# Kernel tuning notes

Hardware: AMD Instinct MI355X
Metric: run time of the kernel (lower is better)

Reference implementation:

```python
import jax, jax.numpy as jnp
import numpy as np

B, LQ, LD = 64, 20, 512
D, NB, WIN = 300, 11, 5
EQ, ED, DESC, KC = 5, 10, 20, 10
VW, VE, VC = 50000, 10000, 5000

# KNRM kernel centers / widths (requires_grad=False buffers in the original)
MU = jnp.array([1.0, 0.9, 0.7, 0.5, 0.3, 0.1, -0.1, -0.3, -0.5, -0.7, -0.9], jnp.float32)
SIGMA = jnp.array([1e-3] + [0.1] * 10, jnp.float32)


def setup_inputs() -> dict:
    key = jax.random.key(0)
    ks = jax.random.split(key, 20)
    f = lambda k, s, sc: jax.random.normal(k, s, jnp.float32) * sc
    return {
        "inputs_qwt": jax.random.randint(ks[0], (B, LQ), 0, VW),
        "inputs_qwm": jnp.ones((B, LQ), jnp.float32),
        "inputs_qei": jax.random.randint(ks[1], (B, EQ), 0, VE),
        "inputs_qet": jax.random.randint(ks[2], (B, EQ * DESC), 0, VW),
        "inputs_qew": jax.random.randint(ks[3], (B, EQ * KC), 0, VC),
        "inputs_qem": jnp.ones((B, EQ), jnp.float32),
        "inputs_dwt": jax.random.randint(ks[4], (B, LD), 0, VW),
        "inputs_dwm": jnp.ones((B, LD), jnp.float32),
        "inputs_dei": jax.random.randint(ks[5], (B, ED), 0, VE),
        "inputs_det": jax.random.randint(ks[6], (B, ED * DESC), 0, VW),
        "inputs_dew": jax.random.randint(ks[7], (B, ED * KC), 0, VC),
        "inputs_dem": jnp.ones((B, ED), jnp.float32),
        "wrd_emb": f(ks[8], (VW, D), 0.1),
        "ent_emb": f(ks[9], (VE, 128), 0.1),
        "car_emb": f(ks[10], (VC, 128), 0.1),
        "bow_W": f(ks[11], (128, D), 0.05), "bow_b": jnp.zeros((128,), jnp.float32),
        "conv_uni_W": f(ks[12], (128, 1, D), 0.05), "conv_uni_b": jnp.zeros((128,), jnp.float32),
        "conv_bi_W": f(ks[13], (128, 2, D), 0.04), "conv_bi_b": jnp.zeros((128,), jnp.float32),
        "conv_tri_W": f(ks[14], (128, 3, D), 0.03), "conv_tri_b": jnp.zeros((128,), jnp.float32),
        "conv_des_W": f(ks[15], (128, WIN, D), 0.02), "conv_des_b": jnp.zeros((128,), jnp.float32),
        "dense_f_W": f(ks[16], (1, 16 * NB), 0.1), "dense_f_b": jnp.zeros((1,), jnp.float32),
    }


def _conv_words(x, w, b):
    # x: [N, L, D]; w: [O, k, D] -> relu conv over the word axis, valid padding -> [N, L-k+1, O]
    k, L = w.shape[1], x.shape[1]
    segs = jnp.stack([x[:, i:L - k + 1 + i] for i in range(k)], axis=2)  # [N, L-k+1, k, D]
    return jax.nn.relu(jnp.einsum('nlkd,okd->nlo', segs, w) + b)


def _l2(x):
    return x / jnp.maximum(jnp.linalg.norm(x, axis=-1, keepdims=True), 1e-10)


def _kernel_pool(q, d, mq, md):
    # q:[B,Lq,128] d:[B,Ld,128] mq:[B,Lq] md:[B,Ld] -> [B, NB]
    sim = jnp.einsum('bqe,bde->bqd', q, d)
    pv = jnp.exp(-0.5 * (sim[..., None] - MU) ** 2 / (SIGMA ** 2)) * md[:, None, :, None]
    lps = jnp.log(jnp.maximum(pv.sum(2), 1e-10)) * 0.01 * mq[:, :, None]
    return lps.sum(1)


def _forward(inputs_qwt, inputs_qwm, inputs_qei, inputs_qet, inputs_qew, inputs_qem,
             inputs_dwt, inputs_dwm, inputs_dei, inputs_det, inputs_dew, inputs_dem,
             wrd_emb, ent_emb, car_emb, bow_W, bow_b,
             conv_uni_W, conv_uni_b, conv_bi_W, conv_bi_b, conv_tri_W, conv_tri_b,
             conv_des_W, conv_des_b, dense_f_W, dense_f_b):
    b = inputs_qwt.shape[0]
    qw = wrd_emb[inputs_qwt]  # [B, LQ, D]
    dw = wrd_emb[inputs_dwt]  # [B, LD, D]

    def ent_branch(ids_e, ids_desc, ids_car, n_ent, w_bow):
        desc = wrd_emb[ids_desc].reshape(b * n_ent, DESC, D)
        e_conv = _conv_words(desc, conv_des_W, conv_des_b).max(1).reshape(b, n_ent, 128)
        t = car_emb[ids_car].reshape(b, n_ent * KC, 128)
        att = jax.nn.softmax((w_bow * t).sum(2).reshape(b, n_ent, KC, 1), axis=2)
        ew = (att * t.reshape(b, n_ent, KC, 128)).sum(2)
        return ent_emb[ids_e] + e_conv + ew

    qw_bow = (jnp.einsum('bld,od->blo', qw, bow_W) + bow_b).sum(1, keepdims=True)  # [B,1,128]
    dw_bow = (jnp.einsum('bld,od->blo', dw, bow_W) + bow_b).sum(1, keepdims=True)
    qs = _l2(ent_branch(inputs_qei, inputs_qet, inputs_qew, EQ, qw_bow))  # [B,5,128]
    ds = _l2(ent_branch(inputs_dei, inputs_det, inputs_dew, ED, dw_bow))  # [B,10,128]

    qu = _l2(_conv_words(qw, conv_uni_W, conv_uni_b))
    qb = _l2(_conv_words(qw, conv_bi_W, conv_bi_b))
    qt = _l2(_conv_words(qw, conv_tri_W, conv_tri_b))
    du = _l2(_conv_words(dw, conv_uni_W, conv_uni_b))
    db = _l2(_conv_words(dw, conv_bi_W, conv_bi_b))
    dt = _l2(_conv_words(dw, conv_tri_W, conv_tri_b))

    mqu, mqb, mqt = inputs_qwm, inputs_qwm[:, :-1], inputs_qwm[:, :-2]
    mdu, mdb, mdt = inputs_dwm, inputs_dwm[:, :-1], inputs_dwm[:, :-2]

    kp = _kernel_pool
    pools = [kp(qu, du, mqu, mdu), kp(qu, dt, mqu, mdt), kp(qu, db, mqu, mdb),
             kp(qb, du, mqb, mdu), kp(qt, du, mqt, mdu), kp(qb, db, mqb, mdb),
             kp(qb, dt, mqb, mdt), kp(qt, db, mqt, mdb), kp(qt, dt, mqt, mdt),
             kp(qs, du, inputs_qem, mdu), kp(qs, db, inputs_qem, mdb), kp(qs, dt, inputs_qem, mdt),
             kp(qu, ds, mqu, inputs_dem), kp(qb, ds, mqb, inputs_dem), kp(qt, ds, mqt, inputs_dem),
             kp(qs, ds, inputs_qem, inputs_dem)]
    feats = jnp.concatenate(pools, axis=1)  # [B, 16*NB]
    return jnp.tanh(feats @ dense_f_W.T + dense_f_b)[:, 0]


def reference(inputs_qwt, inputs_qwm, inputs_qei, inputs_qet, inputs_qew, inputs_qem,
              inputs_dwt, inputs_dwm, inputs_dei, inputs_det, inputs_dew, inputs_dem,
              wrd_emb, ent_emb, car_emb, bow_W, bow_b,
              conv_uni_W, conv_uni_b, conv_bi_W, conv_bi_b, conv_tri_W, conv_tri_b,
              conv_des_W, conv_des_b, dense_f_W, dense_f_b):
    return _forward(inputs_qwt, inputs_qwm, inputs_qei, inputs_qet, inputs_qew, inputs_qem,
                    inputs_dwt, inputs_dwm, inputs_dei, inputs_det, inputs_dew, inputs_dem,
                    wrd_emb, ent_emb, car_emb, bow_W, bow_b,
                    conv_uni_W, conv_uni_b, conv_bi_W, conv_bi_b, conv_tri_W, conv_tri_b,
                    conv_des_W, conv_des_b, dense_f_W, dense_f_b)
```

## Files before the change

### kernel.cpp

```cpp
#include <hip/hip_runtime.h>

typedef unsigned short u16;
typedef unsigned int u32;
typedef __attribute__((ext_vector_type(8))) short bf16x8;
typedef __attribute__((ext_vector_type(4))) float f32x4;

#define DEVI __device__ __forceinline__

namespace {
constexpr int LQ_ = 20, LD_ = 512, D_ = 300;
constexpr int EQ_ = 5, ED_ = 10, KC_ = 10;
constexpr int QROWS = 62, DROWS = 1543;
constexpr int QSTR = 64, DSTR = 1600;
constexpr int NCVT = 14649;
constexpr float MU_H[11] = {1.0f,0.9f,0.7f,0.5f,0.3f,0.1f,-0.1f,-0.3f,-0.5f,-0.7f,-0.9f};
}

__constant__ int P2QT_C[16] = {0,0,0,1,2,1,1,2,2,3,3,3,0,1,2,3};
__constant__ int P2DT_C[16] = {0,2,1,0,0,1,2,1,2,0,1,2,3,3,3,3};
__constant__ int NP_C[4]   = {2,2,4,4};
__constant__ int PPL_C[16] = {0,1,0,0, 2,3,0,0, 2,3,4,5, 4,5,6,7};
__constant__ int SETL_C[16]= {0,0,0,0, 0,0,0,0, 1,1,0,0, 1,1,0,0};

DEVI u16 f2bf(float f){ union{float f;u32 u;} v; v.f=f; u32 r=(v.u+0x7fffu+((v.u>>16)&1u))>>16; return (u16)r; }
DEVI float bf2f(u16 h){ union{u32 u;float f;} v; v.u=((u32)h)<<16; return v.f; }

__global__ __launch_bounds__(256) void k_prep(const float* __restrict__ emb, u16* __restrict__ emb16,
                                              const float* __restrict__ Wu, const float* __restrict__ Wb,
                                              const float* __restrict__ Wt, const float* __restrict__ Wd,
                                              u16* __restrict__ Wp){
  const int bx = blockIdx.x;
  if(bx < NCVT){
    long i4 = (long)bx*256 + threadIdx.x;
    if(i4 < 3750000){
      float4 v = ((const float4*)emb)[i4];
      ushort4 o4; o4.x=f2bf(v.x); o4.y=f2bf(v.y); o4.z=f2bf(v.z); o4.w=f2bf(v.w);
      ((ushort4*)emb16)[i4] = o4;
    }
  } else {
    const int b2 = bx - NCVT;
    const int ts = b2/10, ks = b2%10;
    const float* W; int kk, tap;
    if(ts==0){W=Wu;kk=1;tap=0;}
    else if(ts<3){W=Wb;kk=2;tap=ts-1;}
    else if(ts<6){W=Wt;kk=3;tap=ts-3;}
    else {W=Wd;kk=5;tap=ts-6;}
    for(int idx=threadIdx.x; idx<4096; idx+=256){
      int n0=idx>>9, lane=(idx>>3)&63, j=idx&7;
      int col=lane&15, kg=lane>>4;
      int d=ks*32+kg*8+j, o=n0*16+col;
      float v = (d<300)? W[((long)o*kk + tap)*300 + d] : 0.f;
      Wp[(((long)(ts*8+n0)*10+ks)*64 + lane)*8 + j] = f2bf(v);
    }
  }
}

__global__ __launch_bounds__(512) void k_main(
    const int* __restrict__ dwt, const int* __restrict__ qwt,
    const int* __restrict__ qet, const int* __restrict__ det,
    const u16* __restrict__ emb16, const u16* __restrict__ Wp,
    const float* __restrict__ bu, const float* __restrict__ bb, const float* __restrict__ bt,
    const float* __restrict__ bd,
    u16* __restrict__ dcat, u16* __restrict__ qcat,
    float* __restrict__ qdm, float* __restrict__ ddm, float* __restrict__ parts)
{
  __shared__ __align__(16) char smem[77088];
  __shared__ int tokid[80];
  const int bx = blockIdx.x, t = threadIdx.x;
  const int lane=t&63, wave=t>>6, col16=lane&15, kg=lane>>4;
  if(bx < 576){
    const bool isdoc = bx < 512;
    const int seq   = isdoc? (bx>>3) : (bx-512);
    const int l0    = isdoc? (bx&7)*64 : 0;
    const int Ltok  = isdoc? LD_ : LQ_;
    u16* outp = isdoc? dcat : qcat;
    const long seqstride = isdoc? (long)DSTR*128 : (long)QSTR*128;
    u16* xs = (u16*)smem;
    float* ot = (float*)(smem + 43296);
    const int nrows = min(66, Ltok - l0);
    if(t<66) tokid[t] = (t<nrows)? (isdoc? dwt[seq*LD_+l0+t] : qwt[seq*LQ_+t]) : 0;
    __syncthreads();
    #pragma unroll
    for(int it=0; it<11; it++){
      int idx = t + it*512;
      if(idx < 66*80){
        int r=idx/80, q=idx-r*80;
        ushort4 o4;
        if(q<75 && r<nrows) o4 = *(const ushort4*)(emb16 + (long)tokid[r]*300 + q*4);
        else { o4.x=0;o4.y=0;o4.z=0;o4.w=0; }
        *(ushort4*)&xs[r*328 + q*4] = o4;
      }
    }
    __syncthreads();
    #pragma unroll
    for(int c=0;c<3;c++){
      const int tb = (c==0)?0:((c==1)?1:3);
      const int base = (c==0)?0:((c==1)?Ltok:2*Ltok-1);
      const float* bias = (c==0)?bu:((c==1)?bb:bt);
      f32x4 acc4[4];
      #pragma unroll
      for(int mt=0;mt<4;mt++) acc4[mt]=(f32x4){0.f,0.f,0.f,0.f};
      #pragma unroll
      for(int h=0;h<2;h++){
        bf16x8 wf[15];
        #pragma unroll
        for(int i=0;i<=c;i++)
          #pragma unroll
          for(int k5=0;k5<5;k5++)
            wf[i*5+k5] = *(const bf16x8*)(Wp + (((long)((tb+i)*8 + wave)*10) + h*5 + k5)*512 + lane*8);
        #pragma unroll
        for(int mt=0;mt<4;mt++){
          #pragma unroll
          for(int i=0;i<=c;i++){
            const u16* xrow = &xs[(mt*16 + col16 + i)*328 + h*160 + kg*8];
            #pragma unroll
            for(int k5=0;k5<5;k5++){
              bf16x8 a = *(const bf16x8*)(xrow + k5*32);
              acc4[mt]=__builtin_amdgcn_mfma_f32_16x16x32_bf16(a,wf[i*5+k5],acc4[mt],0,0,0);
            }
          }
        }
      }
      const float bv = bias[wave*16+col16];
      #pragma unroll
      for(int mt=0;mt<4;mt++)
        #pragma unroll
        for(int reg=0;reg<4;reg++)
          ot[(mt*16+kg*4+reg)*132 + wave*16+col16] = fmaxf(acc4[mt][reg]+bv, 0.f);
      __syncthreads();
      {
        const int p = t>>3, j = t&7;
        const int nv = min(64, (Ltok - c) - l0);
        float ss=0.f;
        if(p<nv){
          #pragma unroll
          for(int k=0;k<16;k++){ float v = ot[p*132 + j + 8*k]; ss += v*v; }
        }
        ss += __shfl_xor(ss,1); ss += __shfl_xor(ss,2); ss += __shfl_xor(ss,4);
        if(p<nv){
          float inv = 1.0f/fmaxf(sqrtf(ss),1e-10f);
          u16* ob = outp + (long)seq*seqstride + ((long)(base + l0 + p))*128 + j*16;
          #pragma unroll
          for(int hh=0;hh<2;hh++){
            bf16x8 o8;
            #pragma unroll
            for(int e=0;e<8;e++) o8[e] = (short)f2bf(ot[p*132 + j*16 + hh*8 + e]*inv);
            *(bf16x8*)(ob + hh*8) = o8;
          }
        }
      }
      __syncthreads();
    }
    {
      const int nr = isdoc? 64 : 20;
      const int g  = isdoc? (bx&7) : 0;
      const int b  = seq;
      if(t<304){
        float s=0.f;
        if(t<300){
          for(int r=0;r<nr;r++) s += bf2f(xs[r*328 + t]);
        }
        parts[(((long)(isdoc?64:0) + b)*8 + g)*304 + t] = s;
      }
    }
  } else {
    const int d = bx - 576;
    const bool isq = d < 80;
    const int s0 = (isq? d : d-80)*4;
    const int* dt_ = isq? qet : det;
    float* dm = isq? qdm : ddm;
    u16* xs4 = (u16*)smem;
    if(t<80) tokid[t] = dt_[s0*20 + t];
    __syncthreads();
    #pragma unroll
    for(int it=0; it<13; it++){
      int idx = t + it*512;
      if(idx < 80*80){
        int lr=idx/80, q=idx-lr*80;
        ushort4 o4;
        if(q<75) o4 = *(const ushort4*)(emb16 + (long)tokid[lr]*300 + q*4);
        else { o4.x=0;o4.y=0;o4.z=0;o4.w=0; }
        *(ushort4*)&xs4[lr*328 + q*4] = o4;
      }
    }
    __syncthreads();
    f32x4 acc4[4];
    #pragma unroll
    for(int s=0;s<4;s++) acc4[s]=(f32x4){0.f,0.f,0.f,0.f};
    #pragma unroll
    for(int h=0;h<2;h++){
      bf16x8 wf[25];
      #pragma unroll
      for(int tap=0;tap<5;tap++)
        #pragma unroll
        for(int k5=0;k5<5;k5++)
          wf[tap*5+k5] = *(const bf16x8*)(Wp + (((long)((6+tap)*8 + wave)*10) + h*5 + k5)*512 + lane*8);
      #pragma unroll
      for(int s=0;s<4;s++){
        #pragma unroll
        for(int tap=0;tap<5;tap++){
          const u16* xrow = &xs4[(s*20 + col16 + tap)*328 + h*160 + kg*8];
          #pragma unroll
          for(int k5=0;k5<5;k5++){
            bf16x8 a = *(const bf16x8*)(xrow + k5*32);
            acc4[s]=__builtin_amdgcn_mfma_f32_16x16x32_bf16(a,wf[tap*5+k5],acc4[s],0,0,0);
          }
        }
      }
    }
    const float bv = bd[wave*16+col16];
    #pragma unroll
    for(int s=0;s<4;s++){
      float m=-1e30f;
      #pragma unroll
      for(int reg=0;reg<4;reg++) m=fmaxf(m, acc4[s][reg]+bv);
      m=fmaxf(m,__shfl_xor(m,16));
      m=fmaxf(m,__shfl_xor(m,32));
      m=fmaxf(m,0.f);
      if(kg==0) dm[(long)(s0+s)*128 + wave*16+col16]=m;
    }
  }
}

__global__ __launch_bounds__(128) void k_bowmat(const float* __restrict__ parts,
                                                const float* __restrict__ bowW, const float* __restrict__ bowb,
                                                float* __restrict__ qbow, float* __restrict__ dbow){
  const int side = blockIdx.x>>6, b = blockIdx.x&63, t = threadIdx.x;
  __shared__ float sv[304];
  const float* p = parts + (((long)side*64 + b)*8)*304;
  const int ng = side? 8 : 1;
  for(int d=t; d<304; d+=128){
    float s=0.f;
    for(int g=0;g<ng;g++) s += p[g*304+d];
    sv[d]=s;
  }
  __syncthreads();
  float acc=0.f;
  const float* w = bowW + (long)t*D_;
  for(int d=0; d<D_; d++) acc += sv[d]*w[d];
  const float L = side? (float)LD_ : (float)LQ_;
  (side? dbow:qbow)[b*128+t] = acc + L*bowb[t];
}

__global__ __launch_bounds__(256) void k_entpost(
    const int* __restrict__ qei, const int* __restrict__ qew,
    const int* __restrict__ dei, const int* __restrict__ dew,
    const float* __restrict__ qdm, const float* __restrict__ ddm,
    const float* __restrict__ qbow, const float* __restrict__ dbow,
    const float* __restrict__ ent, const float* __restrict__ car,
    u16* __restrict__ qcat, u16* __restrict__ dcat)
{
  const int e15 = blockIdx.x, b = blockIdx.y, t = threadIdx.x;
  const bool isq = (e15 < EQ_);
  const int e = isq? e15 : e15-EQ_;
  const float* dmx = isq? (qdm + (long)(b*EQ_+e)*128) : (ddm + (long)(b*ED_+e)*128);
  const float* bw = isq? (qbow + b*128) : (dbow + b*128);
  const int eid = isq? qei[b*EQ_+e] : dei[b*ED_+e];
  const int* carids = isq? (qew + b*EQ_*KC_ + e*KC_) : (dew + b*ED_*KC_ + e*KC_);
  u16* orow = isq? (qcat + ((long)b*QSTR + 57 + e)*128) : (dcat + ((long)b*DSTR + 1533 + e)*128);

  __shared__ float carS[KC_*128];
  __shared__ float sc[KC_], att[KC_];
  __shared__ float red[4];
  for(int idx=t; idx<KC_*128; idx+=256){
    int j = idx>>7, c = idx&127;
    carS[j*128+c] = car[(long)carids[j]*128 + c];
  }
  __syncthreads();
  {
    const int j = t>>4, l16 = t&15;
    if(j < KC_){
      float s=0.f;
      for(int c=l16;c<128;c+=16) s += bw[c]*carS[j*128+c];
      s += __shfl_xor(s,1); s += __shfl_xor(s,2); s += __shfl_xor(s,4); s += __shfl_xor(s,8);
      if(l16==0) sc[j]=s;
    }
  }
  __syncthreads();
  if(t==0){
    float m=-1e30f;
    for(int x=0;x<KC_;x++) m = fmaxf(m, sc[x]);
    float ssum=0.f;
    for(int x=0;x<KC_;x++){ float e2=__expf(sc[x]-m); att[x]=e2; ssum+=e2; }
    float rs = 1.0f/ssum;
    for(int x=0;x<KC_;x++) att[x]*=rs;
  }
  __syncthreads();
  float val=0.f;
  if(t<128){
    float ew=0.f;
    for(int x=0;x<KC_;x++) ew += att[x]*carS[x*128+t];
    val = ent[(long)eid*128+t] + dmx[t] + ew;
  }
  float ss = val*val;
  ss += __shfl_xor(ss,1); ss += __shfl_xor(ss,2); ss += __shfl_xor(ss,4);
  ss += __shfl_xor(ss,8); ss += __shfl_xor(ss,16); ss += __shfl_xor(ss,32);
  if((t&63)==0) red[t>>6]=ss;
  __syncthreads();
  if(t<128){
    float nv = 1.0f/fmaxf(sqrtf(red[0]+red[1]),1e-10f);
    orow[t] = f2bf(val*nv);
  }
}

__global__ __launch_bounds__(512) void k_simgauss(const u16* __restrict__ qcat, const u16* __restrict__ dcat,
                                                  const float* __restrict__ dwm, const float* __restrict__ dem,
                                                  float* __restrict__ Spart){
  const int b=blockIdx.x, piece=blockIdx.y;
  const int t=threadIdx.x, lane=t&63, wave=t>>6;
  const int qtile=wave>>1, dpar=wave&1;
  const int col16=lane&15, kg=lane>>4;
  constexpr int NT[4]={8,8,8,1};
  constexpr int TBASE[4]={0,8,16,24};
  constexpr int PEND[4]={512,1023,1533,1543};
  bf16x8 afr[4];
  #pragma unroll
  for(int ks=0;ks<4;ks++)
    afr[ks] = *(const bf16x8*)&qcat[((long)b*QSTR + qtile*16+col16)*128 + ks*32 + kg*8];
  float aP[4][11], aS[4][11];
  #pragma unroll
  for(int r=0;r<4;r++)
    #pragma unroll
    for(int m=0;m<11;m++){ aP[r][m]=0.f; aS[r][m]=0.f; }
  const int t0 = dpar*4;
  const int t1 = (NT[piece] < t0+4)? NT[piece] : t0+4;
  for(int tt=t0; tt<t1; tt++){
    const int tb = TBASE[piece]+tt;
    f32x4 acc[4];
    #pragma unroll
    for(int n0=0;n0<4;n0++) acc[n0]=(f32x4){0.f,0.f,0.f,0.f};
    #pragma unroll
    for(int ks=0;ks<4;ks++){
      #pragma unroll
      for(int n0=0;n0<4;n0++){
        bf16x8 bfr = *(const bf16x8*)&dcat[((long)b*DSTR + tb*64 + n0*16+col16)*128 + ks*32 + kg*8];
        acc[n0]=__builtin_amdgcn_mfma_f32_16x16x32_bf16(afr[ks],bfr,acc[n0],0,0,0);
      }
    }
    #pragma unroll
    for(int n0=0;n0<4;n0++){
      const int col = tb*64 + n0*16 + col16;
      float md;
      if(col<512) md = dwm[b*LD_+col];
      else if(col<1023) md = dwm[b*LD_+col-512];
      else if(col<1533) md = dwm[b*LD_+col-1023];
      else if(col<1543) md = dem[b*ED_+(col-1533)];
      else md = 0.f;
      const bool pr = col < PEND[piece];
      const float mdP = pr? md : 0.f;
      const float mdS = pr? 0.f : md;
      #pragma unroll
      for(int reg=0;reg<4;reg++){
        const float svv = acc[n0][reg];
        {
          float d1 = svv-1.0f;
          float e = __expf(-500000.0f*d1*d1);
          aP[reg][0] += mdP*e; aS[reg][0] += mdS*e;
        }
        #pragma unroll
        for(int m=1;m<11;m++){
          float dm = svv-MU_H[m];
          float e = __expf(-50.0f*dm*dm);
          aP[reg][m] += mdP*e; aS[reg][m] += mdS*e;
        }
      }
    }
  }
  #pragma unroll
  for(int reg=0;reg<4;reg++)
    #pragma unroll
    for(int m=0;m<11;m++){
      float vP=aP[reg][m];
      vP+=__shfl_xor(vP,1); vP+=__shfl_xor(vP,2); vP+=__shfl_xor(vP,4); vP+=__shfl_xor(vP,8);
      aP[reg][m]=vP;
      float vS=aS[reg][m];
      vS+=__shfl_xor(vS,1); vS+=__shfl_xor(vS,2); vS+=__shfl_xor(vS,4); vS+=__shfl_xor(vS,8);
      aS[reg][m]=vS;
    }
  if(col16==0){
    #pragma unroll
    for(int reg=0;reg<4;reg++){
      const int qr = qtile*16 + kg*4 + reg;
      float* o = Spart + (((long)b*64 + qr)*8 + piece*2+dpar)*22;
      #pragma unroll
      for(int m=0;m<11;m++){ o[m]=aP[reg][m]; o[11+m]=aS[reg][m]; }
    }
  }
}

__global__ __launch_bounds__(256) void k_feats(const float* __restrict__ Spart, const float* __restrict__ qwm,
                                               const float* __restrict__ qem, const float* __restrict__ dfW,
                                               const float* __restrict__ dfb, float* __restrict__ out){
  const int b = blockIdx.x, t = threadIdx.x;
  __shared__ float fsh[176];
  __shared__ float red[4];
  if(t<176){
    const int pool = t/11, m = t - pool*11;
    const int qt = P2QT_C[pool], dt = P2DT_C[pool];
    const int qlo = (qt==0)?0:((qt==1)?20:((qt==2)?39:57));
    const int qn  = (qt==0)?20:((qt==1)?19:((qt==2)?18:5));
    float f = 0.f;
    for(int r=0;r<qn;r++){
      const int qr = qlo + r;
      float mq = (qt<3)? qwm[b*LQ_+r] : qem[b*EQ_+r];
      const float* row = Spart + (((long)b*64 + qr)*8)*22 + m;
      float sv = 0.f;
      const int np = NP_C[dt];
      for(int k=0;k<np;k++){
        const int ii = dt*4+k;
        sv += row[PPL_C[ii]*22 + SETL_C[ii]*11];
      }
      f += logf(fmaxf(sv,1e-10f))*0.01f*mq;
    }
    fsh[t] = f;
  }
  __syncthreads();
  float v = (t<176)? fsh[t]*dfW[t] : 0.f;
  v += __shfl_xor(v,1); v += __shfl_xor(v,2); v += __shfl_xor(v,4);
  v += __shfl_xor(v,8); v += __shfl_xor(v,16); v += __shfl_xor(v,32);
  if((t&63)==0) red[t>>6]=v;
  __syncthreads();
  if(t==0) out[b] = tanhf(red[0]+red[1]+red[2]+red[3] + dfb[0]);
}

extern "C" void kernel_launch(void* const* d_in, const int* in_sizes, int n_in,
                              void* d_out, int out_size, void* d_ws, size_t ws_size,
                              hipStream_t stream)
{
  const int*   qwt=(const int*)d_in[0];
  const float* qwm=(const float*)d_in[1];
  const int*   qei=(const int*)d_in[2];
  const int*   qet=(const int*)d_in[3];
  const int*   qew=(const int*)d_in[4];
  const float* qem=(const float*)d_in[5];
  const int*   dwt=(const int*)d_in[6];
  const float* dwm=(const float*)d_in[7];
  const int*   dei=(const int*)d_in[8];
  const int*   det=(const int*)d_in[9];
  const int*   dew=(const int*)d_in[10];
  const float* dem=(const float*)d_in[11];
  const float* emb=(const float*)d_in[12];
  const float* ent=(const float*)d_in[13];
  const float* car=(const float*)d_in[14];
  const float* bowW=(const float*)d_in[15];
  const float* bowb=(const float*)d_in[16];
  const float* Wu=(const float*)d_in[17];
  const float* bu=(const float*)d_in[18];
  const float* Wb=(const float*)d_in[19];
  const float* bb=(const float*)d_in[20];
  const float* Wt=(const float*)d_in[21];
  const float* bt=(const float*)d_in[22];
  const float* Wd=(const float*)d_in[23];
  const float* bd=(const float*)d_in[24];
  const float* dfW=(const float*)d_in[25];
  const float* dfb=(const float*)d_in[26];
  float* out=(float*)d_out;

  char* ws=(char*)d_ws;
  size_t off=0;
  auto A=[&](size_t n){ size_t r=off; off=(off+n+255)&~(size_t)255; return r; };
  u16* Wp     = (u16*)(ws + A((size_t)11*8*10*64*8*2));
  u16* dcat   = (u16*)(ws + A((size_t)64*DSTR*128*2));
  u16* qcat   = (u16*)(ws + A((size_t)64*QSTR*128*2));
  float* qdm  = (float*)(ws + A((size_t)320*128*4));
  float* ddm  = (float*)(ws + A((size_t)640*128*4));
  float* parts= (float*)(ws + A((size_t)2*64*8*304*4));
  float* qbow = (float*)(ws + A((size_t)64*128*4));
  float* dbow = (float*)(ws + A((size_t)64*128*4));
  float* Spart= (float*)(ws + A((size_t)64*64*8*22*4));
  u16* emb16  = (u16*)(ws + A((size_t)50000*300*2));
  if(off > ws_size) return;

  k_prep<<<NCVT+110,256,0,stream>>>(emb,emb16,Wu,Wb,Wt,Wd,Wp);
  k_main<<<816,512,0,stream>>>(dwt,qwt,qet,det,emb16,Wp,bu,bb,bt,bd,dcat,qcat,qdm,ddm,parts);
  k_bowmat<<<128,128,0,stream>>>(parts,bowW,bowb,qbow,dbow);
  k_entpost<<<dim3(15,64),256,0,stream>>>(qei,qew,dei,dew,qdm,ddm,qbow,dbow,ent,car,qcat,dcat);
  k_simgauss<<<dim3(64,4),512,0,stream>>>(qcat,dcat,dwm,dem,Spart);
  k_feats<<<64,256,0,stream>>>(Spart,qwm,qem,dfW,dfb,out);
}
```

Before: 155.0 us.

## Compute all three word convs in one pass, alias LDS, fold bow matvec into entpost

```diff
diff --git a/kernel.cpp b/kernel.cpp
--- a/kernel.cpp
+++ b/kernel.cpp
@@ -64,7 +64,7 @@
     u16* __restrict__ dcat, u16* __restrict__ qcat,
     float* __restrict__ qdm, float* __restrict__ ddm, float* __restrict__ parts)
 {
-  __shared__ __align__(16) char smem[77088];
+  __shared__ __align__(16) char smem[52480];
   __shared__ int tokid[80];
   const int bx = blockIdx.x, t = threadIdx.x;
   const int lane=t&63, wave=t>>6, col16=lane&15, kg=lane>>4;
@@ -76,7 +76,7 @@
     u16* outp = isdoc? dcat : qcat;
     const long seqstride = isdoc? (long)DSTR*128 : (long)QSTR*128;
     u16* xs = (u16*)smem;
-    float* ot = (float*)(smem + 43296);
+    float* ot = (float*)smem;
     const int nrows = min(66, Ltok - l0);
     if(t<66) tokid[t] = (t<nrows)? (isdoc? dwt[seq*LD_+l0+t] : qwt[seq*LQ_+t]) : 0;
     __syncthreads();
@@ -92,41 +92,67 @@
       }
     }
     __syncthreads();
+    f32x4 aU[4], aB[4], aT[4];
+    #pragma unroll
+    for(int mt=0;mt<4;mt++){
+      aU[mt]=(f32x4){0.f,0.f,0.f,0.f};
+      aB[mt]=(f32x4){0.f,0.f,0.f,0.f};
+      aT[mt]=(f32x4){0.f,0.f,0.f,0.f};
+    }
+    #pragma unroll
+    for(int h=0;h<2;h++){
+      #pragma unroll
+      for(int i=0;i<3;i++){
+        #pragma unroll
+        for(int k5=0;k5<5;k5++){
+          const long wboff = ((long)h*5 + k5)*512 + lane*8;
+          bf16x8 av[4];
+          #pragma unroll
+          for(int mt=0;mt<4;mt++)
+            av[mt] = *(const bf16x8*)&xs[(mt*16+col16+i)*328 + h*160 + k5*32 + kg*8];
+          {
+            bf16x8 wT = *(const bf16x8*)(Wp + ((long)((3+i)*8+wave)*10)*512 + wboff);
+            #pragma unroll
+            for(int mt=0;mt<4;mt++)
+              aT[mt]=__builtin_amdgcn_mfma_f32_16x16x32_bf16(av[mt],wT,aT[mt],0,0,0);
+          }
+          if(i<2){
+            bf16x8 wB = *(const bf16x8*)(Wp + ((long)((1+i)*8+wave)*10)*512 + wboff);
+            #pragma unroll
+            for(int mt=0;mt<4;mt++)
+              aB[mt]=__builtin_amdgcn_mfma_f32_16x16x32_bf16(av[mt],wB,aB[mt],0,0,0);
+          }
+          if(i==0){
+            bf16x8 wU = *(const bf16x8*)(Wp + ((long)(wave)*10)*512 + wboff);
+            #pragma unroll
+            for(int mt=0;mt<4;mt++)
+              aU[mt]=__builtin_amdgcn_mfma_f32_16x16x32_bf16(av[mt],wU,aU[mt],0,0,0);
+          }
+        }
+      }
+    }
+    if(t<304){
+      const int nr = isdoc? 64 : 20;
+      const int g  = isdoc? (bx&7) : 0;
+      float s=0.f;
+      if(t<300){
+        for(int r=0;r<nr;r++) s += bf2f(xs[r*328 + t]);
+      }
+      parts[(((long)(isdoc?64:0) + seq)*8 + g)*304 + t] = s;
+    }
+    __syncthreads();
     #pragma unroll
     for(int c=0;c<3;c++){
-      const int tb = (c==0)?0:((c==1)?1:3);
       const int base = (c==0)?0:((c==1)?Ltok:2*Ltok-1);
       const float* bias = (c==0)?bu:((c==1)?bb:bt);
-      f32x4 acc4[4];
-      #pragma unroll
-      for(int mt=0;mt<4;mt++) acc4[mt]=(f32x4){0.f,0.f,0.f,0.f};
-      #pragma unroll
-      for(int h=0;h<2;h++){
-        bf16x8 wf[15];
-        #pragma unroll
-        for(int i=0;i<=c;i++)
-          #pragma unroll
-          for(int k5=0;k5<5;k5++)
-            wf[i*5+k5] = *(const bf16x8*)(Wp + (((long)((tb+i)*8 + wave)*10) + h*5 + k5)*512 + lane*8);
-        #pragma unroll
-        for(int mt=0;mt<4;mt++){
-          #pragma unroll
-          for(int i=0;i<=c;i++){
-            const u16* xrow = &xs[(mt*16 + col16 + i)*328 + h*160 + kg*8];
-            #pragma unroll
-            for(int k5=0;k5<5;k5++){
-              bf16x8 a = *(const bf16x8*)(xrow + k5*32);
-              acc4[mt]=__builtin_amdgcn_mfma_f32_16x16x32_bf16(a,wf[i*5+k5],acc4[mt],0,0,0);
-            }
-          }
-        }
-      }
       const float bv = bias[wave*16+col16];
       #pragma unroll
       for(int mt=0;mt<4;mt++)
         #pragma unroll
-        for(int reg=0;reg<4;reg++)
-          ot[(mt*16+kg*4+reg)*132 + wave*16+col16] = fmaxf(acc4[mt][reg]+bv, 0.f);
+        for(int reg=0;reg<4;reg++){
+          float v = (c==0? aU[mt][reg] : (c==1? aB[mt][reg] : aT[mt][reg])) + bv;
+          ot[(mt*16+kg*4+reg)*132 + wave*16+col16] = fmaxf(v, 0.f);
+        }
       __syncthreads();
       {
         const int p = t>>3, j = t&7;
@@ -151,18 +177,6 @@
       }
       __syncthreads();
     }
-    {
-      const int nr = isdoc? 64 : 20;
-      const int g  = isdoc? (bx&7) : 0;
-      const int b  = seq;
-      if(t<304){
-        float s=0.f;
-        if(t<300){
-          for(int r=0;r<nr;r++) s += bf2f(xs[r*328 + t]);
-        }
-        parts[(((long)(isdoc?64:0) + b)*8 + g)*304 + t] = s;
-      }
-    }
   } else {
     const int d = bx - 576;
     const bool isq = d < 80;
@@ -222,31 +236,11 @@
   }
 }
 
-__global__ __launch_bounds__(128) void k_bowmat(const float* __restrict__ parts,
-                                                const float* __restrict__ bowW, const float* __restrict__ bowb,
-                                                float* __restrict__ qbow, float* __restrict__ dbow){
-  const int side = blockIdx.x>>6, b = blockIdx.x&63, t = threadIdx.x;
-  __shared__ float sv[304];
-  const float* p = parts + (((long)side*64 + b)*8)*304;
-  const int ng = side? 8 : 1;
-  for(int d=t; d<304; d+=128){
-    float s=0.f;
-    for(int g=0;g<ng;g++) s += p[g*304+d];
-    sv[d]=s;
-  }
-  __syncthreads();
-  float acc=0.f;
-  const float* w = bowW + (long)t*D_;
-  for(int d=0; d<D_; d++) acc += sv[d]*w[d];
-  const float L = side? (float)LD_ : (float)LQ_;
-  (side? dbow:qbow)[b*128+t] = acc + L*bowb[t];
-}
-
 __global__ __launch_bounds__(256) void k_entpost(
     const int* __restrict__ qei, const int* __restrict__ qew,
     const int* __restrict__ dei, const int* __restrict__ dew,
     const float* __restrict__ qdm, const float* __restrict__ ddm,
-    const float* __restrict__ qbow, const float* __restrict__ dbow,
+    const float* __restrict__ parts, const float* __restrict__ bowW, const float* __restrict__ bowb,
     const float* __restrict__ ent, const float* __restrict__ car,
     u16* __restrict__ qcat, u16* __restrict__ dcat)
 {
@@ -254,24 +248,42 @@
   const bool isq = (e15 < EQ_);
   const int e = isq? e15 : e15-EQ_;
   const float* dmx = isq? (qdm + (long)(b*EQ_+e)*128) : (ddm + (long)(b*ED_+e)*128);
-  const float* bw = isq? (qbow + b*128) : (dbow + b*128);
   const int eid = isq? qei[b*EQ_+e] : dei[b*ED_+e];
   const int* carids = isq? (qew + b*EQ_*KC_ + e*KC_) : (dew + b*ED_*KC_ + e*KC_);
   u16* orow = isq? (qcat + ((long)b*QSTR + 57 + e)*128) : (dcat + ((long)b*DSTR + 1533 + e)*128);
 
   __shared__ float carS[KC_*128];
+  __shared__ float sv[304];
+  __shared__ float bwS[128];
   __shared__ float sc[KC_], att[KC_];
   __shared__ float red[4];
+  const float* p = parts + (((long)(isq?0:64) + b)*8)*304;
+  const int ng = isq? 1 : 8;
+  for(int d=t; d<304; d+=256){
+    float s=0.f;
+    for(int g=0;g<ng;g++) s += p[g*304+d];
+    sv[d]=s;
+  }
   for(int idx=t; idx<KC_*128; idx+=256){
     int j = idx>>7, c = idx&127;
     carS[j*128+c] = car[(long)carids[j]*128 + c];
+  }
+  __syncthreads();
+  {
+    const int ch = t>>1, h = t&1;
+    float acc=0.f;
+    const float* w = bowW + (long)ch*300 + h*150;
+    const float* x = sv + h*150;
+    for(int d=0; d<150; d++) acc += x[d]*w[d];
+    acc += __shfl_xor(acc,1);
+    if(h==0) bwS[ch] = acc + (isq? (float)LQ_ : (float)LD_)*bowb[ch];
   }
   __syncthreads();
   {
     const int j = t>>4, l16 = t&15;
     if(j < KC_){
       float s=0.f;
-      for(int c=l16;c<128;c+=16) s += bw[c]*carS[j*128+c];
+      for(int c=l16;c<128;c+=16) s += bwS[c]*carS[j*128+c];
       s += __shfl_xor(s,1); s += __shfl_xor(s,2); s += __shfl_xor(s,4); s += __shfl_xor(s,8);
       if(l16==0) sc[j]=s;
     }
@@ -465,16 +477,13 @@
   float* qdm  = (float*)(ws + A((size_t)320*128*4));
   float* ddm  = (float*)(ws + A((size_t)640*128*4));
   float* parts= (float*)(ws + A((size_t)2*64*8*304*4));
-  float* qbow = (float*)(ws + A((size_t)64*128*4));
-  float* dbow = (float*)(ws + A((size_t)64*128*4));
   float* Spart= (float*)(ws + A((size_t)64*64*8*22*4));
   u16* emb16  = (u16*)(ws + A((size_t)50000*300*2));
   if(off > ws_size) return;
 
   k_prep<<<NCVT+110,256,0,stream>>>(emb,emb16,Wu,Wb,Wt,Wd,Wp);
   k_main<<<816,512,0,stream>>>(dwt,qwt,qet,det,emb16,Wp,bu,bb,bt,bd,dcat,qcat,qdm,ddm,parts);
-  k_bowmat<<<128,128,0,stream>>>(parts,bowW,bowb,qbow,dbow);
-  k_entpost<<<dim3(15,64),256,0,stream>>>(qei,qew,dei,dew,qdm,ddm,qbow,dbow,ent,car,qcat,dcat);
+  k_entpost<<<dim3(15,64),256,0,stream>>>(qei,qew,dei,dew,qdm,ddm,parts,bowW,bowb,ent,car,qcat,dcat);
   k_simgauss<<<dim3(64,4),512,0,stream>>>(qcat,dcat,dwm,dem,Spart);
   k_feats<<<64,256,0,stream>>>(Spart,qwm,qem,dfW,dfb,out);
 }
```

Result: slower. 168.5 us (+8.7%).
